# Performance work log

Measured on AMD Instinct MI355X. Metric: run time of the kernel, lower is better.

## Reference

```python
import jax, jax.numpy as jnp
import numpy as np

B, K, C = 8192, 64, 8  # batch, feature dim, number of private-attribute classes


def setup_inputs() -> dict:
    key = jax.random.key(0)
    k1, k2, k3 = jax.random.split(key, 3)
    mu = jax.random.normal(k1, (B, K), dtype=jnp.float32)
    private_attribute = jax.random.randint(k2, (B,), 0, C)
    A = jax.random.normal(k3, (K, K), dtype=jnp.float32) * 0.05
    cov = A @ A.T + jnp.eye(K, dtype=jnp.float32)  # SPD prior covariance
    return {"mu": mu, "private_attribute": private_attribute, "cov": cov}


def _kldiv(mu1, S1, mu2, S2, k):
    # KL( N(mu1,S1) || N(mu2,S2) )
    d = mu2 - mu1
    tr = jnp.trace(jnp.linalg.solve(S2, S1))       # tr(inv(S2) S1)
    quad = d @ jnp.linalg.solve(S2, d)             # d^T inv(S2) d
    ld2 = jnp.linalg.slogdet(S2)[1]
    ld1 = jnp.linalg.slogdet(S1)[1]
    return 0.5 * (tr + quad - k + ld2 - ld1)


def reference(mu, private_attribute, cov):
    Bn, k = mu.shape
    labels = private_attribute
    ones = jnp.ones((Bn,), mu.dtype)
    counts = jax.ops.segment_sum(ones, labels, num_segments=C)                # [C]
    safe = jnp.maximum(counts, 1.0)
    mu_F = jax.ops.segment_sum(mu, labels, num_segments=C) / safe[:, None]    # [C,k] group means
    mu_total = jnp.mean(mu, axis=0)                                           # [k]
    dt = mu - mu_total
    Sigma_total = cov + dt.T @ dt / Bn                                        # [k,k]
    dc = mu - mu_F[labels]                                                    # [B,k]
    outer = jnp.einsum('bi,bj->bij', dc, dc)                                  # [B,k,k]
    Sigma_F = cov + jax.ops.segment_sum(outer, labels, num_segments=C) / safe[:, None, None]  # [C,k,k]
    kl = jax.vmap(lambda m, S: _kldiv(m, S, mu_total, Sigma_total, k))(mu_F, Sigma_F)  # [C]
    # The original loops `for i in range(len(keys)-1)` over dict keys ordered by
    # first occurrence in the batch, i.e. it SKIPS the class whose first sample
    # appears latest. Reproduce that exactly.
    pos = jnp.arange(Bn)
    first_pos = jnp.min(
        jnp.where(labels[:, None] == jnp.arange(C)[None, :], pos[:, None], Bn), axis=0
    )                                                                          # [C]
    present = first_pos < Bn
    last_key = jnp.argmax(jnp.where(present, first_pos, -1))
    w = jnp.where(present & (jnp.arange(C) != last_key), counts, 0.0)          # count_Fs weights
    result = jnp.sum(kl * w * Bn) / (Bn ** 2)
    return result
```

## Files before the change

### kernel.cpp

```cpp
#include <hip/hip_runtime.h>

#define CC 8
#define KK 64
#define BB 8192
#define NCHUNK 16
#define NGBLK (NCHUNK * CC)
#define ROWS_PER_CHUNK (BB / NCHUNK)

#define OFF_GPART 0
#define OFF_SPART 2097152
#define OFF_CPART 2129920
#define OFF_FPART 2130432
#define OFF_GT    2130944
#define OFF_INV   2163712
#define OFF_LD2   2196480
#define OFF_TERMS 2196488
#define OFF_CNTR  2196552
#define OFF_RDY   2196556
#define OFF_FLG   2196560

#define SM_BUFA  0
#define SM_BUFB  4160
#define SM_PANEL 8320
#define SM_LB    8832
#define SM_LDI   12992
#define SM_MB    13056
#define SM_INTS  13120
#define SMEM_BACK 13128

__device__ __forceinline__ double readlane_f64(double v, int lane) {
  union { double d; int i[2]; } u, r;
  u.d = v;
  r.i[0] = __builtin_amdgcn_readlane(u.i[0], lane);
  r.i[1] = __builtin_amdgcn_readlane(u.i[1], lane);
  return r.d;
}

__global__ __launch_bounds__(256) void k_front(const float* __restrict__ mu,
                                               const int* __restrict__ labels, char* ws) {
  __shared__ double smem[2176];
  int blk = blockIdx.x;
  int chunk = blk >> 3, c = blk & 7;
  int tid = threadIdx.x;
  int lane = tid & 63, w = tid >> 6;
  int tx = tid & 15, ty = tid >> 4;
  float* rows = (float*)smem;
  int* labs = (int*)(smem + 2048);
  float* ssum = (float*)(smem + 2080);
  int* scnt = (int*)(smem + 2112);
  int* sfst = (int*)(smem + 2114);
  float* Gpart = (float*)(ws + OFF_GPART);
  float* Spart = (float*)(ws + OFF_SPART);
  int* cpart = (int*)(ws + OFF_CPART);
  int* fpart = (int*)(ws + OFF_FPART);
  if (blk == 0) {
    double* GT = (double*)(ws + OFF_GT);
    for (int i = tid; i < KK * KK; i += 256) GT[i] = 0.0;
    if (tid == 0) {
      *(int*)(ws + OFF_CNTR) = 0;
      *(int*)(ws + OFF_RDY) = 0;
      *(int*)(ws + OFF_FLG) = 0;
    }
  }

  double acc[4][4] = {{0.0}};
  float rsum = 0.f;
  int cnt = 0, first = BB;
  int base = chunk * ROWS_PER_CHUNK;
  const float4* mu4 = (const float4*)mu + (size_t)base * (KK / 4);
  if (tid < KK) ssum[tid] = 0.f;

  float4 pf[4];
  int plab = 0;
#pragma unroll
  for (int i = 0; i < 4; ++i) pf[i] = mu4[tid + i * 256];
  if (tid < 64) plab = labels[base + tid];

#pragma unroll 1
  for (int g = 0; g < ROWS_PER_CHUNK / 64; ++g) {
    __syncthreads();
    float4* rows4 = (float4*)rows;
#pragma unroll
    for (int i = 0; i < 4; ++i) rows4[tid + i * 256] = pf[i];
    if (tid < 64) labs[tid] = plab;
    __syncthreads();
    if (g + 1 < ROWS_PER_CHUNK / 64) {
#pragma unroll
      for (int i = 0; i < 4; ++i) pf[i] = mu4[(g + 1) * 1024 + tid + i * 256];
      if (tid < 64) plab = labels[base + (g + 1) * 64 + tid];
    }
#pragma unroll 4
    for (int r = 0; r < 16; ++r) {
      int rr = w * 16 + r;
      if (labs[rr] == c) rsum += rows[rr * KK + lane];
    }
    if (lane < 16 && labs[w * 16 + lane] == c) {
      cnt++;
      first = min(first, base + g * 64 + w * 16 + lane);
    }
    unsigned long long m = __ballot(labs[lane] == c);
    while (m) {
      int r = __builtin_ctzll(m);
      m &= m - 1;
      const float4* rw4 = (const float4*)(rows + r * KK);
      float4 a4 = rw4[ty], b4 = rw4[tx];
      const float* ai = (const float*)&a4;
      const float* bj = (const float*)&b4;
#pragma unroll
      for (int a = 0; a < 4; ++a)
#pragma unroll
        for (int b = 0; b < 4; ++b) acc[a][b] += (double)ai[a] * (double)bj[b];
    }
  }
  int slot = chunk * CC + c;
  float* Gp = Gpart + (size_t)slot * KK * KK;
#pragma unroll
  for (int a = 0; a < 4; ++a) {
    float4 v = make_float4((float)acc[a][0], (float)acc[a][1], (float)acc[a][2], (float)acc[a][3]);
    *(float4*)(Gp + (ty * 4 + a) * KK + tx * 4) = v;
  }
  atomicAdd(&ssum[lane], rsum);
#pragma unroll
  for (int off = 32; off; off >>= 1) {
    cnt += __shfl_down(cnt, off);
    first = min(first, __shfl_down(first, off));
  }
  if (lane == 0) { scnt[w] = cnt; sfst[w] = first; }
  __syncthreads();
  if (tid < KK) Spart[(size_t)slot * KK + tid] = ssum[tid];
  if (tid == 0) {
    cpart[slot] = scnt[0] + scnt[1] + scnt[2] + scnt[3];
    fpart[slot] = min(min(sfst[0], sfst[1]), min(sfst[2], sfst[3]));
  }
}

__device__ __noinline__ double chol64(double* smem, bool isS2) {
  int tid = threadIdx.x;
  int t = tid & 63, w = tid >> 6;
  double (*bufA)[KK + 1] = (double (*)[KK + 1])(smem + SM_BUFA);
  double (*bufB)[KK + 1] = (double (*)[KK + 1])(smem + SM_BUFB);
  double (*panelb)[KK] = (double (*)[KK])(smem + SM_PANEL);
  double (*Lb)[KK + 1] = (double (*)[KK + 1])(smem + SM_LB);
  double* Ldi = smem + SM_LDI;
  double (*cur)[KK + 1] = bufA;
  double (*nxt)[KK + 1] = bufB;
  double ldacc = 0.0;
  int bound = t | 7;
#pragma unroll 1
  for (int p = 0; p < 8; ++p) {
    const int P0 = p * 8;
    double cc_[8];
#pragma unroll
    for (int m = 0; m < 8; ++m) cc_[m] = cur[t][P0 + m];
    double uu[8];
    double pd = 1.0;
#pragma unroll
    for (int m = 0; m < 8; ++m) {
      double akk = readlane_f64(cc_[m], P0 + m);
      pd *= akk;
      double inv;
      asm("v_rcp_f64 %0, %1" : "=v"(inv) : "v"(akk));
      inv = inv * fma(-akk, inv, 2.0);
      uu[m] = cc_[m] * inv;
      if (w == 0) {
        panelb[m][t] = cc_[m];
        if (isS2) {
          double rsv = sqrt(akk) * inv;
          Lb[t][P0 + m] = cc_[m] * rsv;
          if (t == 0) Ldi[P0 + m] = rsv;
        }
      }
#pragma unroll
      for (int mm = m + 1; mm < 8; ++mm)
        cc_[mm] -= uu[m] * readlane_f64(cc_[m], P0 + mm);
    }
    ldacc += log(pd);
    __syncthreads();
#pragma unroll 1
    for (int jb = p + 1 + w; jb < 8; jb += 4) {
      int j = jb * 8;
      if (j <= bound) {
        double aj[8];
#pragma unroll
        for (int q = 0; q < 8; ++q) aj[q] = cur[t][j + q];
#pragma unroll
        for (int m = 0; m < 8; ++m)
#pragma unroll
          for (int q = 0; q < 8; ++q) aj[q] -= uu[m] * panelb[m][j + q];
#pragma unroll
        for (int q = 0; q < 8; ++q) nxt[t][j + q] = aj[q];
      }
    }
    __syncthreads();
    { auto tmp = cur; cur = nxt; nxt = tmp; }
  }
  return ldacc;
}

__global__ __launch_bounds__(256) void k_back(const float* __restrict__ cov,
                                              float* out, char* ws) {
  __shared__ double smem[SMEM_BACK];
  int blk = blockIdx.x;
  int tid = threadIdx.x;
  int t = tid & 63, w = tid >> 6;
  float* Gpart = (float*)(ws + OFF_GPART);
  float* Spart = (float*)(ws + OFF_SPART);
  int* cpart = (int*)(ws + OFF_CPART);
  int* fpart = (int*)(ws + OFF_FPART);
  double* GT = (double*)(ws + OFF_GT);
  double* invS2 = (double*)(ws + OFF_INV);
  double* ld2g = (double*)(ws + OFF_LD2);
  double* terms = (double*)(ws + OFF_TERMS);
  int* cntr = (int*)(ws + OFF_CNTR);
  int* rdy = (int*)(ws + OFF_RDY);
  int* flg = (int*)(ws + OFF_FLG);
  double* red = smem + SM_BUFB;
  double* mb = smem + SM_MB;
  int* cnt8s = (int*)(smem + SM_INTS);
  int* fst8s = cnt8s + 8;
  const float4* cov4 = (const float4*)cov;

  if (blk < CC) {
    int c = blk;
    if (tid < 64) {
      double so = 0.0, st = 0.0;
#pragma unroll 8
      for (int slot = 0; slot < 128; ++slot) {
        double v = (double)Spart[slot * KK + t];
        st += v;
        if ((slot & 7) == c) so += v;
      }
      smem[SM_MB + t] = so;
      smem[SM_LDI + t] = st;
    } else if (tid < 72) {
      int j = tid - 64;
      int ct = 0, ff = BB;
#pragma unroll
      for (int p = 0; p < NCHUNK; ++p) {
        ct += cpart[p * CC + j];
        ff = min(ff, fpart[p * CC + j]);
      }
      cnt8s[j] = ct;
      fst8s[j] = ff;
    }
    __syncthreads();
    int nc = cnt8s[c];
    double ncd = (double)nc;
    double safe = nc > 0 ? ncd : 1.0;
    double inv_safe = 1.0 / safe;
    if (tid < 64) {
      double m = smem[SM_MB + t] * inv_safe;
      double mt2 = smem[SM_LDI + t] * (1.0 / (double)BB);
      smem[SM_MB + t] = m;
      smem[SM_LDI + t] = mt2 - m;
    }
    __syncthreads();

    double* stash = smem + SM_LB;
#pragma unroll 1
    for (int q = 0; q < 4; ++q) {
      int base_e = tid * 16 + q * 4;
      double s0 = 0.0, s1 = 0.0, s2 = 0.0, s3 = 0.0;
#pragma unroll
      for (int p = 0; p < NCHUNK; ++p) {
        float4 v = ((const float4*)(Gpart + (size_t)(p * CC + c) * KK * KK))[base_e >> 2];
        s0 += (double)v.x; s1 += (double)v.y; s2 += (double)v.z; s3 += (double)v.w;
      }
      int r = base_e >> 6, c0 = base_e & 63;
      float4 cv = cov4[base_e >> 2];
      double mr = mb[r] * ncd;
      double v0 = (double)cv.x + (s0 - mr * mb[c0]) * inv_safe;
      double v1 = (double)cv.y + (s1 - mr * mb[c0 + 1]) * inv_safe;
      double v2 = (double)cv.z + (s2 - mr * mb[c0 + 2]) * inv_safe;
      double v3 = (double)cv.w + (s3 - mr * mb[c0 + 3]) * inv_safe;
      double* ba = smem + SM_BUFA + r * (KK + 1) + c0;
      ba[0] = v0; ba[1] = v1; ba[2] = v2; ba[3] = v3;
      double* sb = stash + r * (KK + 1) + c0;
      sb[0] = v0; sb[1] = v1; sb[2] = v2; sb[3] = v3;
      atomicAdd(&GT[base_e], s0);
      atomicAdd(&GT[base_e + 1], s1);
      atomicAdd(&GT[base_e + 2], s2);
      atomicAdd(&GT[base_e + 3], s3);
    }
    __syncthreads();
    if (tid == 0) {
      __threadfence();
      atomicAdd(rdy, 1);
    }

    double ld1 = chol64(smem, false);

    if (tid == 0) {
      int it = 0;
      while (__hip_atomic_load(flg, __ATOMIC_ACQUIRE, __HIP_MEMORY_SCOPE_AGENT) == 0 &&
             ++it < (1 << 20))
        __builtin_amdgcn_s_sleep(8);
    }
    __syncthreads();
    double ld2 = __hip_atomic_load(ld2g, __ATOMIC_RELAXED, __HIP_MEMORY_SCOPE_AGENT);
    double* dvv = smem + SM_LDI;
    double trp = 0.0, qp = 0.0;
#pragma unroll 4
    for (int rr = 0; rr < 16; ++rr) {
      int r = w * 16 + rr;
      double iv = __hip_atomic_load(&invS2[r * KK + t], __ATOMIC_RELAXED,
                                    __HIP_MEMORY_SCOPE_AGENT);
      trp += iv * stash[r * (KK + 1) + t];
      qp += iv * dvv[r];
    }
    qp *= dvv[t];
#pragma unroll
    for (int m = 32; m; m >>= 1) {
      trp += __shfl_down(trp, m);
      qp += __shfl_down(qp, m);
    }
    double* wred = smem + SM_PANEL;
    if (t == 0) { wred[w * 2] = trp; wred[w * 2 + 1] = qp; }
    __syncthreads();
    if (tid == 0) {
      double tr = wred[0] + wred[2] + wred[4] + wred[6];
      double quad = wred[1] + wred[3] + wred[5] + wred[7];
      int best = 0;
      long long bv = -2;
      for (int j = 0; j < CC; ++j) {
        long long v = cnt8s[j] > 0 ? (long long)fst8s[j] : -1;
        if (v > bv) { bv = v; best = j; }
      }
      double kl = 0.5 * (tr + quad - (double)KK + ld2 - ld1);
      double wgt = (nc > 0 && c != best) ? ncd : 0.0;
      double term = kl * wgt / (double)BB;
      atomicExch((unsigned long long*)&terms[c],
                 (unsigned long long)__double_as_longlong(term));
      __threadfence();
      int old = atomicAdd(cntr, 1);
      if (old == CC - 1) {
        double s = 0.0;
        for (int j = 0; j < CC; ++j) s += atomicAdd(&terms[j], 0.0);
        out[0] = (float)s;
      }
    }
  } else {
    {
      double s = 0.0;
#pragma unroll 8
      for (int p = 0; p < 32; ++p) s += (double)Spart[(w * 32 + p) * KK + t];
      red[w * KK + t] = s;
    }
    __syncthreads();
    if (tid < 64)
      mb[t] = (red[t] + red[KK + t] + red[2 * KK + t] + red[3 * KK + t]) / (double)BB;
    if (tid == 0) {
      int it = 0;
      while (__hip_atomic_load(rdy, __ATOMIC_ACQUIRE, __HIP_MEMORY_SCOPE_AGENT) < CC &&
             ++it < (1 << 20))
        __builtin_amdgcn_s_sleep(8);
    }
    __syncthreads();
    const double invB = 1.0 / (double)BB;
#pragma unroll 1
    for (int q = 0; q < 4; ++q) {
      int base_e = tid * 16 + q * 4;
      int r = base_e >> 6, c0 = base_e & 63;
      float4 cv = cov4[base_e >> 2];
      double mr = mb[r];
      double g0 = __hip_atomic_load(&GT[base_e], __ATOMIC_RELAXED, __HIP_MEMORY_SCOPE_AGENT);
      double g1 = __hip_atomic_load(&GT[base_e + 1], __ATOMIC_RELAXED, __HIP_MEMORY_SCOPE_AGENT);
      double g2 = __hip_atomic_load(&GT[base_e + 2], __ATOMIC_RELAXED, __HIP_MEMORY_SCOPE_AGENT);
      double g3 = __hip_atomic_load(&GT[base_e + 3], __ATOMIC_RELAXED, __HIP_MEMORY_SCOPE_AGENT);
      double* ba = smem + SM_BUFA + r * (KK + 1) + c0;
      ba[0] = (double)cv.x + g0 * invB - mr * mb[c0];
      ba[1] = (double)cv.y + g1 * invB - mr * mb[c0 + 1];
      ba[2] = (double)cv.z + g2 * invB - mr * mb[c0 + 2];
      ba[3] = (double)cv.w + g3 * invB - mr * mb[c0 + 3];
    }
    __syncthreads();
    double ld2 = chol64(smem, true);
    double (*Xs)[KK] = (double (*)[KK])(smem + SM_BUFA);
    if (w == 0) {
      double (*Lb)[KK + 1] = (double (*)[KK + 1])(smem + SM_LB);
      double* Ldi = smem + SM_LDI;
#pragma unroll 1
      for (int g = 0; g < 8; ++g) {
        int I0 = g * 8;
        double sv[8];
#pragma unroll
        for (int m = 0; m < 8; ++m) sv[m] = 0.0;
#pragma unroll 2
        for (int j = 0; j < I0; ++j) {
          double xj = Xs[j][t];
#pragma unroll
          for (int m = 0; m < 8; ++m) sv[m] += Lb[I0 + m][j] * xj;
        }
#pragma unroll
        for (int m = 0; m < 8; ++m) {
          int i = I0 + m;
          double x = (((i == t) ? 1.0 : 0.0) - sv[m]) * Ldi[i];
#pragma unroll
          for (int mm = m + 1; mm < 8; ++mm) sv[mm] += Lb[I0 + mm][i] * x;
          Xs[i][t] = x;
        }
      }
    }
    __syncthreads();
#pragma unroll 1
    for (int rr = 0; rr < 16; ++rr) {
      int r = w + rr * 4;
      int k0 = r > t ? r : t;
      double s = 0.0;
#pragma unroll 2
      for (int k = k0; k < KK; ++k) s += Xs[k][r] * Xs[k][t];
      __hip_atomic_store(&invS2[r * KK + t], s, __ATOMIC_RELAXED, __HIP_MEMORY_SCOPE_AGENT);
    }
    __syncthreads();
    if (tid == 0) {
      __hip_atomic_store(ld2g, ld2, __ATOMIC_RELAXED, __HIP_MEMORY_SCOPE_AGENT);
      __threadfence();
      __hip_atomic_store(flg, 1, __ATOMIC_RELEASE, __HIP_MEMORY_SCOPE_AGENT);
    }
  }
}

extern "C" void kernel_launch(void* const* d_in, const int* in_sizes, int n_in,
                              void* d_out, int out_size, void* d_ws, size_t ws_size,
                              hipStream_t stream) {
  (void)in_sizes; (void)n_in; (void)out_size; (void)ws_size;
  const float* mu = (const float*)d_in[0];
  const int* labels = (const int*)d_in[1];
  const float* cov = (const float*)d_in[2];
  float* out = (float*)d_out;
  char* ws = (char*)d_ws;

  k_front<<<NGBLK, 256, 0, stream>>>(mu, labels, ws);
  k_back<<<CC + 1, 256, 0, stream>>>(cov, out, ws);
}
```

Measured before the change: 125.8 us.

## Reduce per-chunk partials with global atomics instead of workspace slots

The front kernel now accumulates each class Gram matrix, feature sums, counts and first positions directly into global buffers with fp64/int atomics, replacing the per-chunk partial buffers that the back kernel previously summed. The back kernel's Sigma_total block now sums the eight class Gram matrices itself, removing the spin-wait on a ready counter. Two hipMemsetAsync calls are added to zero the accumulators and initialize the first-position minima. This is meant to cut the 2MB partial write/read traffic and the cross-block dependency, at the cost of heavy fp64 atomic contention (16 chunks per address) and extra memset launches.

```diff
diff --git a/kernel.cpp b/kernel.cpp
--- a/kernel.cpp
+++ b/kernel.cpp
@@ -7,17 +7,15 @@
 #define NGBLK (NCHUNK * CC)
 #define ROWS_PER_CHUNK (BB / NCHUNK)
 
-#define OFF_GPART 0
-#define OFF_SPART 2097152
-#define OFF_CPART 2129920
-#define OFF_FPART 2130432
-#define OFF_GT    2130944
-#define OFF_INV   2163712
-#define OFF_LD2   2196480
-#define OFF_TERMS 2196488
-#define OFF_CNTR  2196552
-#define OFF_RDY   2196556
-#define OFF_FLG   2196560
+#define OFF_G     0
+#define OFF_GSUM  262144
+#define OFF_GCNT  264192
+#define OFF_CNTR  264224
+#define OFF_FLG   264228
+#define OFF_GFST  264232
+#define OFF_INV   264264
+#define OFF_LD2   297032
+#define OFF_TERMS 297040
 
 #define SM_BUFA  0
 #define SM_BUFB  4160
@@ -49,19 +47,10 @@
   float* ssum = (float*)(smem + 2080);
   int* scnt = (int*)(smem + 2112);
   int* sfst = (int*)(smem + 2114);
-  float* Gpart = (float*)(ws + OFF_GPART);
-  float* Spart = (float*)(ws + OFF_SPART);
-  int* cpart = (int*)(ws + OFF_CPART);
-  int* fpart = (int*)(ws + OFF_FPART);
-  if (blk == 0) {
-    double* GT = (double*)(ws + OFF_GT);
-    for (int i = tid; i < KK * KK; i += 256) GT[i] = 0.0;
-    if (tid == 0) {
-      *(int*)(ws + OFF_CNTR) = 0;
-      *(int*)(ws + OFF_RDY) = 0;
-      *(int*)(ws + OFF_FLG) = 0;
-    }
-  }
+  double* G = (double*)(ws + OFF_G);
+  float* gsum = (float*)(ws + OFF_GSUM);
+  int* gcount = (int*)(ws + OFF_GCNT);
+  int* gfirst = (int*)(ws + OFF_GFST);
 
   double acc[4][4] = {{0.0}};
   float rsum = 0.f;
@@ -112,13 +101,12 @@
         for (int b = 0; b < 4; ++b) acc[a][b] += (double)ai[a] * (double)bj[b];
     }
   }
-  int slot = chunk * CC + c;
-  float* Gp = Gpart + (size_t)slot * KK * KK;
-#pragma unroll
-  for (int a = 0; a < 4; ++a) {
-    float4 v = make_float4((float)acc[a][0], (float)acc[a][1], (float)acc[a][2], (float)acc[a][3]);
-    *(float4*)(Gp + (ty * 4 + a) * KK + tx * 4) = v;
-  }
+  double* Gc = G + (size_t)c * KK * KK;
+#pragma unroll
+  for (int a = 0; a < 4; ++a)
+#pragma unroll
+    for (int b = 0; b < 4; ++b)
+      atomicAdd(&Gc[(ty * 4 + a) * KK + tx * 4 + b], acc[a][b]);
   atomicAdd(&ssum[lane], rsum);
 #pragma unroll
   for (int off = 32; off; off >>= 1) {
@@ -127,10 +115,16 @@
   }
   if (lane == 0) { scnt[w] = cnt; sfst[w] = first; }
   __syncthreads();
-  if (tid < KK) Spart[(size_t)slot * KK + tid] = ssum[tid];
+  if (tid < KK) {
+    float v = ssum[tid];
+    if (v != 0.f) atomicAdd(&gsum[c * KK + tid], v);
+  }
   if (tid == 0) {
-    cpart[slot] = scnt[0] + scnt[1] + scnt[2] + scnt[3];
-    fpart[slot] = min(min(sfst[0], sfst[1]), min(sfst[2], sfst[3]));
+    int ct = scnt[0] + scnt[1] + scnt[2] + scnt[3];
+    if (ct) {
+      atomicAdd(&gcount[c], ct);
+      atomicMin(&gfirst[c], min(min(sfst[0], sfst[1]), min(sfst[2], sfst[3])));
+    }
   }
 }
 
@@ -203,45 +197,31 @@
   int blk = blockIdx.x;
   int tid = threadIdx.x;
   int t = tid & 63, w = tid >> 6;
-  float* Gpart = (float*)(ws + OFF_GPART);
-  float* Spart = (float*)(ws + OFF_SPART);
-  int* cpart = (int*)(ws + OFF_CPART);
-  int* fpart = (int*)(ws + OFF_FPART);
-  double* GT = (double*)(ws + OFF_GT);
+  double* G = (double*)(ws + OFF_G);
+  float* gsum = (float*)(ws + OFF_GSUM);
+  int* gcount = (int*)(ws + OFF_GCNT);
+  int* gfirst = (int*)(ws + OFF_GFST);
   double* invS2 = (double*)(ws + OFF_INV);
   double* ld2g = (double*)(ws + OFF_LD2);
   double* terms = (double*)(ws + OFF_TERMS);
   int* cntr = (int*)(ws + OFF_CNTR);
-  int* rdy = (int*)(ws + OFF_RDY);
   int* flg = (int*)(ws + OFF_FLG);
-  double* red = smem + SM_BUFB;
   double* mb = smem + SM_MB;
   int* cnt8s = (int*)(smem + SM_INTS);
   int* fst8s = cnt8s + 8;
-  const float4* cov4 = (const float4*)cov;
 
   if (blk < CC) {
     int c = blk;
     if (tid < 64) {
-      double so = 0.0, st = 0.0;
-#pragma unroll 8
-      for (int slot = 0; slot < 128; ++slot) {
-        double v = (double)Spart[slot * KK + t];
-        st += v;
-        if ((slot & 7) == c) so += v;
-      }
-      smem[SM_MB + t] = so;
-      smem[SM_LDI + t] = st;
-    } else if (tid < 72) {
+      double st = 0.0;
+#pragma unroll
+      for (int cc2 = 0; cc2 < CC; ++cc2) st += (double)gsum[cc2 * KK + t];
+      smem[SM_LDI + t] = st * (1.0 / (double)BB);
+      smem[SM_MB + t] = (double)gsum[c * KK + t];
+    } else if (tid < 80) {
       int j = tid - 64;
-      int ct = 0, ff = BB;
-#pragma unroll
-      for (int p = 0; p < NCHUNK; ++p) {
-        ct += cpart[p * CC + j];
-        ff = min(ff, fpart[p * CC + j]);
-      }
-      cnt8s[j] = ct;
-      fst8s[j] = ff;
+      if (j < 8) cnt8s[j] = gcount[j];
+      else fst8s[j - 8] = gfirst[j - 8];
     }
     __syncthreads();
     int nc = cnt8s[c];
@@ -250,43 +230,22 @@
     double inv_safe = 1.0 / safe;
     if (tid < 64) {
       double m = smem[SM_MB + t] * inv_safe;
-      double mt2 = smem[SM_LDI + t] * (1.0 / (double)BB);
       smem[SM_MB + t] = m;
-      smem[SM_LDI + t] = mt2 - m;
+      smem[SM_LDI + t] -= m;
     }
     __syncthreads();
 
     double* stash = smem + SM_LB;
-#pragma unroll 1
-    for (int q = 0; q < 4; ++q) {
-      int base_e = tid * 16 + q * 4;
-      double s0 = 0.0, s1 = 0.0, s2 = 0.0, s3 = 0.0;
-#pragma unroll
-      for (int p = 0; p < NCHUNK; ++p) {
-        float4 v = ((const float4*)(Gpart + (size_t)(p * CC + c) * KK * KK))[base_e >> 2];
-        s0 += (double)v.x; s1 += (double)v.y; s2 += (double)v.z; s3 += (double)v.w;
-      }
-      int r = base_e >> 6, c0 = base_e & 63;
-      float4 cv = cov4[base_e >> 2];
-      double mr = mb[r] * ncd;
-      double v0 = (double)cv.x + (s0 - mr * mb[c0]) * inv_safe;
-      double v1 = (double)cv.y + (s1 - mr * mb[c0 + 1]) * inv_safe;
-      double v2 = (double)cv.z + (s2 - mr * mb[c0 + 2]) * inv_safe;
-      double v3 = (double)cv.w + (s3 - mr * mb[c0 + 3]) * inv_safe;
-      double* ba = smem + SM_BUFA + r * (KK + 1) + c0;
-      ba[0] = v0; ba[1] = v1; ba[2] = v2; ba[3] = v3;
-      double* sb = stash + r * (KK + 1) + c0;
-      sb[0] = v0; sb[1] = v1; sb[2] = v2; sb[3] = v3;
-      atomicAdd(&GT[base_e], s0);
-      atomicAdd(&GT[base_e + 1], s1);
-      atomicAdd(&GT[base_e + 2], s2);
-      atomicAdd(&GT[base_e + 3], s3);
-    }
-    __syncthreads();
-    if (tid == 0) {
-      __threadfence();
-      atomicAdd(rdy, 1);
-    }
+    const double* Gc = G + (size_t)c * KK * KK;
+#pragma unroll
+    for (int q = 0; q < 16; ++q) {
+      int e = tid + q * 256;
+      int r = e >> 6, c0 = e & 63;
+      double v = (double)cov[e] + (Gc[e] - ncd * mb[r] * mb[c0]) * inv_safe;
+      smem[SM_BUFA + r * (KK + 1) + c0] = v;
+      stash[r * (KK + 1) + c0] = v;
+    }
+    __syncthreads();
 
     double ld1 = chol64(smem, false);
 
@@ -340,38 +299,22 @@
       }
     }
   } else {
-    {
-      double s = 0.0;
-#pragma unroll 8
-      for (int p = 0; p < 32; ++p) s += (double)Spart[(w * 32 + p) * KK + t];
-      red[w * KK + t] = s;
-    }
-    __syncthreads();
-    if (tid < 64)
-      mb[t] = (red[t] + red[KK + t] + red[2 * KK + t] + red[3 * KK + t]) / (double)BB;
-    if (tid == 0) {
-      int it = 0;
-      while (__hip_atomic_load(rdy, __ATOMIC_ACQUIRE, __HIP_MEMORY_SCOPE_AGENT) < CC &&
-             ++it < (1 << 20))
-        __builtin_amdgcn_s_sleep(8);
+    if (tid < 64) {
+      double st = 0.0;
+#pragma unroll
+      for (int cc2 = 0; cc2 < CC; ++cc2) st += (double)gsum[cc2 * KK + t];
+      mb[t] = st * (1.0 / (double)BB);
     }
     __syncthreads();
     const double invB = 1.0 / (double)BB;
 #pragma unroll 1
-    for (int q = 0; q < 4; ++q) {
-      int base_e = tid * 16 + q * 4;
-      int r = base_e >> 6, c0 = base_e & 63;
-      float4 cv = cov4[base_e >> 2];
-      double mr = mb[r];
-      double g0 = __hip_atomic_load(&GT[base_e], __ATOMIC_RELAXED, __HIP_MEMORY_SCOPE_AGENT);
-      double g1 = __hip_atomic_load(&GT[base_e + 1], __ATOMIC_RELAXED, __HIP_MEMORY_SCOPE_AGENT);
-      double g2 = __hip_atomic_load(&GT[base_e + 2], __ATOMIC_RELAXED, __HIP_MEMORY_SCOPE_AGENT);
-      double g3 = __hip_atomic_load(&GT[base_e + 3], __ATOMIC_RELAXED, __HIP_MEMORY_SCOPE_AGENT);
-      double* ba = smem + SM_BUFA + r * (KK + 1) + c0;
-      ba[0] = (double)cv.x + g0 * invB - mr * mb[c0];
-      ba[1] = (double)cv.y + g1 * invB - mr * mb[c0 + 1];
-      ba[2] = (double)cv.z + g2 * invB - mr * mb[c0 + 2];
-      ba[3] = (double)cv.w + g3 * invB - mr * mb[c0 + 3];
+    for (int q = 0; q < 16; ++q) {
+      int e = tid + q * 256;
+      double g = 0.0;
+#pragma unroll
+      for (int c2 = 0; c2 < CC; ++c2) g += G[(size_t)c2 * KK * KK + e];
+      int r = e >> 6, c0 = e & 63;
+      smem[SM_BUFA + r * (KK + 1) + c0] = (double)cov[e] + g * invB - mb[r] * mb[c0];
     }
     __syncthreads();
     double ld2 = chol64(smem, true);
@@ -430,6 +373,9 @@
   float* out = (float*)d_out;
   char* ws = (char*)d_ws;
 
+  hipMemsetAsync(ws, 0, OFF_GFST, stream);
+  hipMemsetAsync(ws + OFF_GFST, 0x7f, CC * sizeof(int), stream);
+
   k_front<<<NGBLK, 256, 0, stream>>>(mu, labels, ws);
   k_back<<<CC + 1, 256, 0, stream>>>(cov, out, ws);
 }
```

New measurement: 129.6 us. 3.0% more time.
